# Kernel optimization log

Hardware: AMD Instinct MI355X
Metric: run time of the kernel (lower is better)

The kernel has to match this reference:

```python
import jax, jax.numpy as jnp
import numpy as np

N = 50000      # nodes
E = 800000     # edges
D = 128        # input_dim
HID = 128      # hidden_dim
OUT = 128      # output_dim
NH = 16        # n_heads (head_dim = 8)
EF = 16        # edge_feat_dim
RF = 64        # r_feat_dim
KV = 2 * D + EF + RF  # 336


def _ln(x, g, b):
    m = x.mean(-1, keepdims=True)
    v = ((x - m) ** 2).mean(-1, keepdims=True)
    return (x - m) / jnp.sqrt(v + 1e-5) * g + b


def _mlp(x, W1, b1, g, be, W2, b2):
    # Linear -> LayerNorm -> ReLU -> Linear (targetdiff-style MLP, norm=True)
    h = jax.nn.relu(_ln(x @ W1 + b1, g, be))
    return h @ W2 + b2


def setup_inputs() -> dict:
    key = jax.random.key(0)
    ks = jax.random.split(key, 32)

    def w(k, shape, fan_in):
        return (jax.random.normal(k, shape, jnp.float32) / np.sqrt(fan_in)).astype(jnp.float32)

    inp = {
        'h': jax.random.normal(ks[0], (N, D), jnp.float32),
        'rel_x': jax.random.normal(ks[1], (E, 3), jnp.float32),
        'r_feat': jax.random.normal(ks[2], (E, RF), jnp.float32),
        'edge_feat': jax.random.normal(ks[3], (E, EF), jnp.float32),
        'edge_index': jax.random.randint(ks[4], (2, E), 0, N, jnp.int64 if jax.config.jax_enable_x64 else jnp.int32),
        # xk MLP: KV -> HID -> OUT
        'xk_W1': w(ks[5], (KV, HID), KV), 'xk_b1': jnp.zeros((HID,), jnp.float32),
        'xk_g': jnp.ones((HID,), jnp.float32), 'xk_be': jnp.zeros((HID,), jnp.float32),
        'xk_W2': w(ks[6], (HID, OUT), HID), 'xk_b2': jnp.zeros((OUT,), jnp.float32),
        # xv MLP: KV -> HID -> NH
        'xv_W1': w(ks[7], (KV, HID), KV), 'xv_b1': jnp.zeros((HID,), jnp.float32),
        'xv_g': jnp.ones((HID,), jnp.float32), 'xv_be': jnp.zeros((HID,), jnp.float32),
        'xv_W2': w(ks[8], (HID, NH), HID), 'xv_b2': jnp.zeros((NH,), jnp.float32),
        # xq MLP: D -> HID -> OUT
        'xq_W1': w(ks[9], (D, HID), D), 'xq_b1': jnp.zeros((HID,), jnp.float32),
        'xq_g': jnp.ones((HID,), jnp.float32), 'xq_be': jnp.zeros((HID,), jnp.float32),
        'xq_W2': w(ks[10], (HID, OUT), HID), 'xq_b2': jnp.zeros((OUT,), jnp.float32),
        # edge-weight net: Linear(RF,1) + sigmoid
        'ew_W': w(ks[11], (RF, 1), RF), 'ew_b': jnp.zeros((1,), jnp.float32),
    }
    return inp


def reference(h, rel_x, r_feat, edge_feat, edge_index,
              xk_W1, xk_b1, xk_g, xk_be, xk_W2, xk_b2,
              xv_W1, xv_b1, xv_g, xv_be, xv_W2, xv_b2,
              xq_W1, xq_b1, xq_g, xq_be, xq_W2, xq_b2,
              ew_W, ew_b):
    src, dst = edge_index[0], edge_index[1]
    # gather -> MLPs
    kv_input = jnp.concatenate([edge_feat, r_feat, h[dst], h[src]], axis=-1)  # [E, KV]
    k = _mlp(kv_input, xk_W1, xk_b1, xk_g, xk_be, xk_W2, xk_b2).reshape(-1, NH, OUT // NH)
    v = _mlp(kv_input, xv_W1, xv_b1, xv_g, xv_be, xv_W2, xv_b2)              # [E, NH]
    e_w = jax.nn.sigmoid(r_feat @ ew_W + ew_b)                               # [E, 1]
    v = v * e_w
    v = v[:, :, None] * rel_x[:, None, :]                                    # [E, NH, 3]
    q = _mlp(h, xq_W1, xq_b1, xq_g, xq_be, xq_W2, xq_b2).reshape(-1, NH, OUT // NH)
    # scatter-softmax over dst segments
    s = (q[dst] * k).sum(-1) / np.sqrt(OUT // NH)                            # [E, NH]
    smax = jax.ops.segment_max(s, dst, num_segments=N)
    ex = jnp.exp(s - smax[dst])
    den = jax.ops.segment_sum(ex, dst, num_segments=N)
    alpha = ex / den[dst]                                                     # [E, NH]
    m = alpha[:, :, None] * v                                                 # [E, NH, 3]
    out = jax.ops.segment_sum(m, dst, num_segments=N)                         # [N, NH, 3]
    return out.mean(1)                                                        # [N, 3]
```

## Files before the change

### kernel.cpp

```cpp
#include <hip/hip_runtime.h>
#include <hip/hip_bf16.h>

#define NN 50000
#define NE 800000
#define DD 128
#define NHD 16
#define EFD 16
#define RFD 64
#define KVD 336
#define KP  352
#define KST 360
#define ME 64
#define HPAD 132

typedef __attribute__((ext_vector_type(8))) short bf16x8;
typedef __attribute__((ext_vector_type(4))) float f32x4;

__device__ __forceinline__ unsigned short f2bf(float f) {
    __hip_bfloat16 h = __float2bfloat16(f);
    return __builtin_bit_cast(unsigned short, h);
}
__device__ __forceinline__ float bf2f(unsigned short u) {
    return __uint_as_float(((unsigned)u) << 16);
}

__global__ __launch_bounds__(256) void prep_wt(
    const float* __restrict__ xkW1, const float* __restrict__ xvW1,
    unsigned short* __restrict__ Wt)
{
    const int n = blockIdx.x;
    const float* W = (n < 128) ? xkW1 : xvW1;
    const int col = n & 127;
    for (int k = threadIdx.x; k < KST; k += 256) {
        float v = (k < KVD) ? W[(size_t)k * 128 + col] : 0.0f;
        Wt[(size_t)n * KST + k] = f2bf(v);
    }
}

__global__ __launch_bounds__(256) void prep_hbf(
    const float* __restrict__ h, unsigned short* __restrict__ hb)
{
    const size_t i = ((size_t)blockIdx.x * 256 + threadIdx.x) * 4;
    const float4 f = *(const float4*)&h[i];
    ushort4 o;
    o.x = f2bf(f.x); o.y = f2bf(f.y); o.z = f2bf(f.z); o.w = f2bf(f.w);
    *(ushort4*)&hb[i] = o;
}

__global__ __launch_bounds__(128) void qmlp_kernel(
    const float* __restrict__ h,
    const float* __restrict__ W1, const float* __restrict__ b1,
    const float* __restrict__ g,  const float* __restrict__ be,
    const float* __restrict__ W2, const float* __restrict__ b2,
    unsigned short* __restrict__ q_bf)
{
    __shared__ float hs[4][DD];
    __shared__ float hid[4][DD];
    __shared__ float red[4][2][2];
    const int j  = threadIdx.x;
    const int n0 = blockIdx.x * 4;

    #pragma unroll
    for (int n = 0; n < 4; n++) hs[n][j] = h[(size_t)(n0 + n) * DD + j];
    __syncthreads();

    float a[4];
    #pragma unroll
    for (int n = 0; n < 4; n++) a[n] = b1[j];
    #pragma unroll 8
    for (int i = 0; i < DD; i++) {
        float w = W1[i * DD + j];
        #pragma unroll
        for (int n = 0; n < 4; n++) a[n] = fmaf(hs[n][i], w, a[n]);
    }

    const int wid = j >> 6;
    #pragma unroll
    for (int n = 0; n < 4; n++) {
        float s1 = a[n], s2 = a[n] * a[n];
        #pragma unroll
        for (int off = 32; off > 0; off >>= 1) {
            s1 += __shfl_xor(s1, off);
            s2 += __shfl_xor(s2, off);
        }
        if ((j & 63) == 0) { red[n][0][wid] = s1; red[n][1][wid] = s2; }
    }
    __syncthreads();

    const float gg = g[j], bb = be[j];
    #pragma unroll
    for (int n = 0; n < 4; n++) {
        float s1   = red[n][0][0] + red[n][0][1];
        float s2   = red[n][1][0] + red[n][1][1];
        float mean = s1 * (1.0f / DD);
        float var  = s2 * (1.0f / DD) - mean * mean;
        float r    = (a[n] - mean) * rsqrtf(var + 1e-5f) * gg + bb;
        hid[n][j]  = fmaxf(r, 0.0f);
    }
    __syncthreads();

    float o[4];
    #pragma unroll
    for (int n = 0; n < 4; n++) o[n] = b2[j];
    #pragma unroll 8
    for (int i = 0; i < DD; i++) {
        float w = W2[i * DD + j];
        #pragma unroll
        for (int n = 0; n < 4; n++) o[n] = fmaf(hid[n][i], w, o[n]);
    }
    #pragma unroll
    for (int n = 0; n < 4; n++) q_bf[(size_t)(n0 + n) * DD + j] = f2bf(o[n]);
}

union SharedU {
    unsigned short kv[ME * KST];
    float hid[ME * HPAD];
};

__global__ __launch_bounds__(256, 3) void edge_kernel(
    const unsigned short* __restrict__ h_bf,
    const float* __restrict__ rel_x,
    const float* __restrict__ r_feat,
    const float* __restrict__ edge_feat,
    const int*   __restrict__ e_src,
    const int*   __restrict__ e_dst,
    const unsigned short* __restrict__ Wt,
    const float* __restrict__ xk_b1, const float* __restrict__ xk_g,
    const float* __restrict__ xk_be,
    const float* __restrict__ xk_W2, const float* __restrict__ xk_b2,
    const float* __restrict__ xv_b1, const float* __restrict__ xv_g,
    const float* __restrict__ xv_be,
    const float* __restrict__ xv_W2, const float* __restrict__ xv_b2,
    const float* __restrict__ ew_W,  const float* __restrict__ ew_b,
    const unsigned short* __restrict__ q_bf,
    float* __restrict__ accN)
{
    __shared__ SharedU u;
    __shared__ float v_s[ME][NHD];
    __shared__ float ew_s[ME];
    __shared__ float rel_s[ME][3];
    __shared__ int   dst_s[ME];
    __shared__ int   src_s[ME];

    const int tid = threadIdx.x;
    const int e0  = blockIdx.x * ME;

    if (tid < ME) { dst_s[tid] = e_dst[e0 + tid]; src_s[tid] = e_src[e0 + tid]; }
    else {
        int t = tid - ME;
        rel_s[t / 3][t % 3] = rel_x[(size_t)e0 * 3 + t];
    }
    __syncthreads();

    {
        const int e = tid >> 2, p = tid & 3;
        const size_t ge = (size_t)(e0 + e);
        {
            float4 f = *(const float4*)&edge_feat[ge * EFD + p * 4];
            ushort4 o; o.x = f2bf(f.x); o.y = f2bf(f.y); o.z = f2bf(f.z); o.w = f2bf(f.w);
            *(ushort4*)&u.kv[e * KST + p * 4] = o;
        }
        {
            float part = 0.0f;
            #pragma unroll
            for (int i = 0; i < 4; i++) {
                float4 f = *(const float4*)&r_feat[ge * RFD + p * 16 + i * 4];
                float4 w = *(const float4*)&ew_W[p * 16 + i * 4];
                part += f.x * w.x + f.y * w.y + f.z * w.z + f.w * w.w;
                ushort4 o; o.x = f2bf(f.x); o.y = f2bf(f.y); o.z = f2bf(f.z); o.w = f2bf(f.w);
                *(ushort4*)&u.kv[e * KST + 16 + p * 16 + i * 4] = o;
            }
            part += __shfl_xor(part, 1);
            part += __shfl_xor(part, 2);
            if (p == 0) ew_s[e] = 1.0f / (1.0f + expf(-(part + ew_b[0])));
        }
        {
            const uint4* hp = (const uint4*)&h_bf[(size_t)dst_s[e] * DD + p * 32];
            uint4* op = (uint4*)&u.kv[e * KST + 80 + p * 32];
            #pragma unroll
            for (int i = 0; i < 4; i++) op[i] = hp[i];
        }
        {
            const uint4* hp = (const uint4*)&h_bf[(size_t)src_s[e] * DD + p * 32];
            uint4* op = (uint4*)&u.kv[e * KST + 208 + p * 32];
            #pragma unroll
            for (int i = 0; i < 4; i++) op[i] = hp[i];
        }
        if (p < 2) {
            uint4 z = make_uint4(0, 0, 0, 0);
            *(uint4*)&u.kv[e * KST + 336 + p * 8] = z;
        }
    }
    __syncthreads();

    const int lane = tid & 63;
    const int wv   = tid >> 6;
    const int half = wv >> 1;
    const int mrow = (wv & 1) * 32;
    const int c15  = lane & 15;
    const int q    = lane >> 4;

    f32x4 acc[2][8];
    #pragma unroll
    for (int mt = 0; mt < 2; mt++)
        #pragma unroll
        for (int nt = 0; nt < 8; nt++) acc[mt][nt] = (f32x4){0.f, 0.f, 0.f, 0.f};

    {
        const unsigned short* WtH = Wt + (size_t)(half * 128 + c15) * KST;
        const unsigned short* kvA = &u.kv[(mrow + c15) * KST];
        for (int ks = 0; ks < 11; ks++) {
            const int k0 = ks * 32 + q * 8;
            bf16x8 a0 = *(const bf16x8*)&kvA[k0];
            bf16x8 a1 = *(const bf16x8*)&kvA[16 * KST + k0];
            #pragma unroll
            for (int nt = 0; nt < 8; nt++) {
                bf16x8 b = *(const bf16x8*)&WtH[(size_t)nt * 16 * KST + k0];
                acc[0][nt] = __builtin_amdgcn_mfma_f32_16x16x32_bf16(a0, b, acc[0][nt], 0, 0, 0);
                acc[1][nt] = __builtin_amdgcn_mfma_f32_16x16x32_bf16(a1, b, acc[1][nt], 0, 0, 0);
            }
        }
    }

    {
        const float* b1p = half ? xv_b1 : xk_b1;
        const float* gp  = half ? xv_g  : xk_g;
        const float* bep = half ? xv_be : xk_be;
        float bia[8], gam[8], bet[8];
        #pragma unroll
        for (int nt = 0; nt < 8; nt++) {
            int idx = nt * 16 + c15;
            bia[nt] = b1p[idx]; gam[nt] = gp[idx]; bet[nt] = bep[idx];
        }
        #pragma unroll
        for (int mt = 0; mt < 2; mt++)
            #pragma unroll
            for (int r = 0; r < 4; r++) {
                float x[8]; float s1 = 0.f, s2 = 0.f;
                #pragma unroll
                for (int nt = 0; nt < 8; nt++) {
                    x[nt] = acc[mt][nt][r] + bia[nt];
                    s1 += x[nt]; s2 = fmaf(x[nt], x[nt], s2);
                }
                #pragma unroll
                for (int off = 1; off < 16; off <<= 1) {
                    s1 += __shfl_xor(s1, off);
                    s2 += __shfl_xor(s2, off);
                }
                float mean = s1 * (1.0f / 128.0f);
                float var  = s2 * (1.0f / 128.0f) - mean * mean;
                float rstd = rsqrtf(var + 1e-5f);
                #pragma unroll
                for (int nt = 0; nt < 8; nt++)
                    acc[mt][nt][r] = fmaxf((x[nt] - mean) * rstd * gam[nt] + bet[nt], 0.0f);
            }
    }
    __syncthreads();

    if (half == 0) {
        #pragma unroll
        for (int mt = 0; mt < 2; mt++)
            #pragma unroll
            for (int r = 0; r < 4; r++)
                #pragma unroll
                for (int nt = 0; nt < 8; nt++)
                    u.hid[(mrow + mt * 16 + q * 4 + r) * HPAD + nt * 16 + c15] = acc[mt][nt][r];
    }
    __syncthreads();

    const int tc2 = tid & 31;
    const int te2 = tid >> 5;
    float k_acc[8][4];
    {
        const float4 b2v = *(const float4*)&xk_b2[tc2 * 4];
        #pragma unroll
        for (int e = 0; e < 8; e++) {
            k_acc[e][0] = b2v.x; k_acc[e][1] = b2v.y;
            k_acc[e][2] = b2v.z; k_acc[e][3] = b2v.w;
        }
        #pragma unroll 4
        for (int i4 = 0; i4 < 32; i4++) {
            const float4 w0 = *(const float4*)&xk_W2[(i4 * 4 + 0) * 128 + tc2 * 4];
            const float4 w1 = *(const float4*)&xk_W2[(i4 * 4 + 1) * 128 + tc2 * 4];
            const float4 w2 = *(const float4*)&xk_W2[(i4 * 4 + 2) * 128 + tc2 * 4];
            const float4 w3 = *(const float4*)&xk_W2[(i4 * 4 + 3) * 128 + tc2 * 4];
            #pragma unroll
            for (int e = 0; e < 8; e++) {
                const float4 hv = *(const float4*)&u.hid[(te2 * 8 + e) * HPAD + i4 * 4];
                k_acc[e][0] = fmaf(hv.x, w0.x, k_acc[e][0]);
                k_acc[e][1] = fmaf(hv.x, w0.y, k_acc[e][1]);
                k_acc[e][2] = fmaf(hv.x, w0.z, k_acc[e][2]);
                k_acc[e][3] = fmaf(hv.x, w0.w, k_acc[e][3]);
                k_acc[e][0] = fmaf(hv.y, w1.x, k_acc[e][0]);
                k_acc[e][1] = fmaf(hv.y, w1.y, k_acc[e][1]);
                k_acc[e][2] = fmaf(hv.y, w1.z, k_acc[e][2]);
                k_acc[e][3] = fmaf(hv.y, w1.w, k_acc[e][3]);
                k_acc[e][0] = fmaf(hv.z, w2.x, k_acc[e][0]);
                k_acc[e][1] = fmaf(hv.z, w2.y, k_acc[e][1]);
                k_acc[e][2] = fmaf(hv.z, w2.z, k_acc[e][2]);
                k_acc[e][3] = fmaf(hv.z, w2.w, k_acc[e][3]);
                k_acc[e][0] = fmaf(hv.w, w3.x, k_acc[e][0]);
                k_acc[e][1] = fmaf(hv.w, w3.y, k_acc[e][1]);
                k_acc[e][2] = fmaf(hv.w, w3.z, k_acc[e][2]);
                k_acc[e][3] = fmaf(hv.w, w3.w, k_acc[e][3]);
            }
        }
    }
    __syncthreads();

    if (half == 1) {
        #pragma unroll
        for (int mt = 0; mt < 2; mt++)
            #pragma unroll
            for (int r = 0; r < 4; r++)
                #pragma unroll
                for (int nt = 0; nt < 8; nt++)
                    u.hid[(mrow + mt * 16 + q * 4 + r) * HPAD + nt * 16 + c15] = acc[mt][nt][r];
    }
    __syncthreads();

    #pragma unroll
    for (int p = 0; p < 4; p++) {
        int item = tid + p * 256;
        int e    = item >> 4;
        int col  = item & 15;
        float a = xv_b2[col];
        #pragma unroll 8
        for (int i4 = 0; i4 < 32; i4++) {
            const float4 hv = *(const float4*)&u.hid[e * HPAD + i4 * 4];
            a = fmaf(hv.x, xv_W2[(i4 * 4 + 0) * 16 + col], a);
            a = fmaf(hv.y, xv_W2[(i4 * 4 + 1) * 16 + col], a);
            a = fmaf(hv.z, xv_W2[(i4 * 4 + 2) * 16 + col], a);
            a = fmaf(hv.w, xv_W2[(i4 * 4 + 3) * 16 + col], a);
        }
        v_s[e][col] = a;
    }
    __syncthreads();

    {
        const float inv_s8 = 0.35355339059327373f;
        const int head = tc2 >> 1;
        const int sub  = tc2 & 1;
        #pragma unroll
        for (int e = 0; e < 8; e++) {
            int el  = te2 * 8 + e;
            int dst = dst_s[el];
            const ushort4 qb = *(const ushort4*)&q_bf[(size_t)dst * DD + tc2 * 4];
            float p = bf2f(qb.x) * k_acc[e][0] + bf2f(qb.y) * k_acc[e][1] +
                      bf2f(qb.z) * k_acc[e][2] + bf2f(qb.w) * k_acc[e][3];
            p += __shfl_xor(p, 1);
            if (sub == 0) {
                float ex = expf(p * inv_s8);
                float vw = v_s[el][head] * ew_s[el] * ex;
                float* base = &accN[(((size_t)dst * NHD) + head) * 4];
                atomicAdd(base + 0, vw * rel_s[el][0]);
                atomicAdd(base + 1, vw * rel_s[el][1]);
                atomicAdd(base + 2, vw * rel_s[el][2]);
                atomicAdd(base + 3, ex);
            }
        }
    }
}

__global__ __launch_bounds__(256) void finalize_kernel(
    const float* __restrict__ accN, float* __restrict__ out)
{
    int n = blockIdx.x * blockDim.x + threadIdx.x;
    if (n >= NN) return;
    float ox = 0.0f, oy = 0.0f, oz = 0.0f;
    #pragma unroll
    for (int hh = 0; hh < NHD; hh++) {
        float4 a = *(const float4*)&accN[(((size_t)n * NHD) + hh) * 4];
        if (a.w > 0.0f) {
            float r = 1.0f / a.w;
            ox = fmaf(a.x, r, ox);
            oy = fmaf(a.y, r, oy);
            oz = fmaf(a.z, r, oz);
        }
    }
    out[n * 3 + 0] = ox * (1.0f / NHD);
    out[n * 3 + 1] = oy * (1.0f / NHD);
    out[n * 3 + 2] = oz * (1.0f / NHD);
}

extern "C" void kernel_launch(void* const* d_in, const int* in_sizes, int n_in,
                              void* d_out, int out_size, void* d_ws, size_t ws_size,
                              hipStream_t stream)
{
    const float* h         = (const float*)d_in[0];
    const float* rel_x     = (const float*)d_in[1];
    const float* r_feat    = (const float*)d_in[2];
    const float* edge_feat = (const float*)d_in[3];
    const int*   e_idx     = (const int*)d_in[4];
    const float* xk_W1 = (const float*)d_in[5];
    const float* xk_b1 = (const float*)d_in[6];
    const float* xk_g  = (const float*)d_in[7];
    const float* xk_be = (const float*)d_in[8];
    const float* xk_W2 = (const float*)d_in[9];
    const float* xk_b2 = (const float*)d_in[10];
    const float* xv_W1 = (const float*)d_in[11];
    const float* xv_b1 = (const float*)d_in[12];
    const float* xv_g  = (const float*)d_in[13];
    const float* xv_be = (const float*)d_in[14];
    const float* xv_W2 = (const float*)d_in[15];
    const float* xv_b2 = (const float*)d_in[16];
    const float* xq_W1 = (const float*)d_in[17];
    const float* xq_b1 = (const float*)d_in[18];
    const float* xq_g  = (const float*)d_in[19];
    const float* xq_be = (const float*)d_in[20];
    const float* xq_W2 = (const float*)d_in[21];
    const float* xq_b2 = (const float*)d_in[22];
    const float* ew_W  = (const float*)d_in[23];
    const float* ew_b  = (const float*)d_in[24];

    float* accN = (float*)d_ws;
    unsigned short* h_bf = (unsigned short*)(accN + (size_t)NN * NHD * 4);
    unsigned short* q_bf = h_bf + (size_t)NN * DD;
    unsigned short* Wt   = q_bf + (size_t)NN * DD;

    hipMemsetAsync(accN, 0, (size_t)NN * NHD * 4 * sizeof(float), stream);

    prep_hbf<<<(NN * DD / 4 + 255) / 256, 256, 0, stream>>>(h, h_bf);
    prep_wt<<<256, 256, 0, stream>>>(xk_W1, xv_W1, Wt);

    qmlp_kernel<<<NN / 4, 128, 0, stream>>>(h, xq_W1, xq_b1, xq_g, xq_be,
                                            xq_W2, xq_b2, q_bf);

    edge_kernel<<<NE / ME, 256, 0, stream>>>(
        h_bf, rel_x, r_feat, edge_feat,
        e_idx, e_idx + NE,
        Wt,
        xk_b1, xk_g, xk_be, xk_W2, xk_b2,
        xv_b1, xv_g, xv_be, xv_W2, xv_b2,
        ew_W, ew_b, q_bf, accN);

    finalize_kernel<<<(NN + 255) / 256, 256, 0, stream>>>(accN, (float*)d_out);
}
```

Before: 1.652 ms.

## Compute xk second linear layer with bf16 MFMA instead of scalar FMAs

The hidden activations for the k and v MLPs are now stored to shared memory as bf16 in separate buffers, so both are written at once and the two-phase store/sync sequence goes away. The 128x128 second k layer now runs on MFMA 16x16x32 bf16 instructions, with a pre-transposed bf16 copy of xk_W2 built by a new prep kernel. k results go through shared memory for the attention-score step. This removes a large scalar FP32 FMA loop but adds bf16 rounding of the hidden activations and an extra shared-memory round trip.

```diff
diff --git a/kernel.cpp b/kernel.cpp
--- a/kernel.cpp
+++ b/kernel.cpp
@@ -8,10 +8,10 @@
 #define EFD 16
 #define RFD 64
 #define KVD 336
-#define KP  352
 #define KST 360
 #define ME 64
-#define HPAD 132
+#define HST 136
+#define KSS 132
 
 typedef __attribute__((ext_vector_type(8))) short bf16x8;
 typedef __attribute__((ext_vector_type(4))) float f32x4;
@@ -35,6 +35,17 @@
         float v = (k < KVD) ? W[(size_t)k * 128 + col] : 0.0f;
         Wt[(size_t)n * KST + k] = f2bf(v);
     }
+}
+
+__global__ __launch_bounds__(128) void prep_wt2(
+    const float* __restrict__ xkW2, const float* __restrict__ xvW2,
+    unsigned short* __restrict__ Wt2)
+{
+    const int n = blockIdx.x;
+    const int k = threadIdx.x;
+    float v = (n < 128) ? xkW2[(size_t)k * 128 + n]
+                        : xvW2[(size_t)k * 16 + (n - 128)];
+    Wt2[(size_t)n * 128 + k] = f2bf(v);
 }
 
 __global__ __launch_bounds__(256) void prep_hbf(
@@ -114,7 +125,11 @@
 
 union SharedU {
     unsigned short kv[ME * KST];
-    float hid[ME * HPAD];
+    struct {
+        unsigned short hidk[ME * HST];
+        unsigned short hidv[ME * HST];
+    } s2;
+    float ks[ME * KSS];
 };
 
 __global__ __launch_bounds__(256, 3) void edge_kernel(
@@ -125,18 +140,18 @@
     const int*   __restrict__ e_src,
     const int*   __restrict__ e_dst,
     const unsigned short* __restrict__ Wt,
+    const unsigned short* __restrict__ Wt2,
     const float* __restrict__ xk_b1, const float* __restrict__ xk_g,
-    const float* __restrict__ xk_be,
-    const float* __restrict__ xk_W2, const float* __restrict__ xk_b2,
+    const float* __restrict__ xk_be, const float* __restrict__ xk_b2,
     const float* __restrict__ xv_b1, const float* __restrict__ xv_g,
-    const float* __restrict__ xv_be,
-    const float* __restrict__ xv_W2, const float* __restrict__ xv_b2,
+    const float* __restrict__ xv_be, const float* __restrict__ xv_W2,
+    const float* __restrict__ xv_b2,
     const float* __restrict__ ew_W,  const float* __restrict__ ew_b,
     const unsigned short* __restrict__ q_bf,
     float* __restrict__ accN)
 {
     __shared__ SharedU u;
-    __shared__ float v_s[ME][NHD];
+    __shared__ float v_s[ME][NHD + 1];
     __shared__ float ew_s[ME];
     __shared__ float rel_s[ME][3];
     __shared__ int   dst_s[ME];
@@ -257,68 +272,46 @@
     }
     __syncthreads();
 
-    if (half == 0) {
+    {
+        unsigned short* hdst = half ? u.s2.hidv : u.s2.hidk;
         #pragma unroll
         for (int mt = 0; mt < 2; mt++)
             #pragma unroll
-            for (int r = 0; r < 4; r++)
+            for (int r = 0; r < 4; r++) {
+                const int row = mrow + mt * 16 + q * 4 + r;
                 #pragma unroll
                 for (int nt = 0; nt < 8; nt++)
-                    u.hid[(mrow + mt * 16 + q * 4 + r) * HPAD + nt * 16 + c15] = acc[mt][nt][r];
-    }
-    __syncthreads();
-
-    const int tc2 = tid & 31;
-    const int te2 = tid >> 5;
-    float k_acc[8][4];
-    {
-        const float4 b2v = *(const float4*)&xk_b2[tc2 * 4];
-        #pragma unroll
-        for (int e = 0; e < 8; e++) {
-            k_acc[e][0] = b2v.x; k_acc[e][1] = b2v.y;
-            k_acc[e][2] = b2v.z; k_acc[e][3] = b2v.w;
-        }
-        #pragma unroll 4
-        for (int i4 = 0; i4 < 32; i4++) {
-            const float4 w0 = *(const float4*)&xk_W2[(i4 * 4 + 0) * 128 + tc2 * 4];
-            const float4 w1 = *(const float4*)&xk_W2[(i4 * 4 + 1) * 128 + tc2 * 4];
-            const float4 w2 = *(const float4*)&xk_W2[(i4 * 4 + 2) * 128 + tc2 * 4];
-            const float4 w3 = *(const float4*)&xk_W2[(i4 * 4 + 3) * 128 + tc2 * 4];
-            #pragma unroll
-            for (int e = 0; e < 8; e++) {
-                const float4 hv = *(const float4*)&u.hid[(te2 * 8 + e) * HPAD + i4 * 4];
-                k_acc[e][0] = fmaf(hv.x, w0.x, k_acc[e][0]);
-                k_acc[e][1] = fmaf(hv.x, w0.y, k_acc[e][1]);
-                k_acc[e][2] = fmaf(hv.x, w0.z, k_acc[e][2]);
-                k_acc[e][3] = fmaf(hv.x, w0.w, k_acc[e][3]);
-                k_acc[e][0] = fmaf(hv.y, w1.x, k_acc[e][0]);
-                k_acc[e][1] = fmaf(hv.y, w1.y, k_acc[e][1]);
-                k_acc[e][2] = fmaf(hv.y, w1.z, k_acc[e][2]);
-                k_acc[e][3] = fmaf(hv.y, w1.w, k_acc[e][3]);
-                k_acc[e][0] = fmaf(hv.z, w2.x, k_acc[e][0]);
-                k_acc[e][1] = fmaf(hv.z, w2.y, k_acc[e][1]);
-                k_acc[e][2] = fmaf(hv.z, w2.z, k_acc[e][2]);
-                k_acc[e][3] = fmaf(hv.z, w2.w, k_acc[e][3]);
-                k_acc[e][0] = fmaf(hv.w, w3.x, k_acc[e][0]);
-                k_acc[e][1] = fmaf(hv.w, w3.y, k_acc[e][1]);
-                k_acc[e][2] = fmaf(hv.w, w3.z, k_acc[e][2]);
-                k_acc[e][3] = fmaf(hv.w, w3.w, k_acc[e][3]);
-            }
-        }
-    }
-    __syncthreads();
-
-    if (half == 1) {
-        #pragma unroll
-        for (int mt = 0; mt < 2; mt++)
-            #pragma unroll
-            for (int r = 0; r < 4; r++)
-                #pragma unroll
-                for (int nt = 0; nt < 8; nt++)
-                    u.hid[(mrow + mt * 16 + q * 4 + r) * HPAD + nt * 16 + c15] = acc[mt][nt][r];
-    }
-    __syncthreads();
-
+                    hdst[row * HST + nt * 16 + c15] = f2bf(acc[mt][nt][r]);
+            }
+    }
+    __syncthreads();
+
+    const int mb2 = (wv & 1) * 32;
+    const int nb2 = (wv >> 1) * 64;
+    f32x4 acck[2][4];
+    #pragma unroll
+    for (int mt = 0; mt < 2; mt++)
+        #pragma unroll
+        for (int nt = 0; nt < 4; nt++) acck[mt][nt] = (f32x4){0.f, 0.f, 0.f, 0.f};
+    {
+        const unsigned short* A0 = &u.s2.hidk[(mb2 + c15) * HST];
+        const unsigned short* A1 = &u.s2.hidk[(mb2 + 16 + c15) * HST];
+        const unsigned short* B0 = &Wt2[(size_t)(nb2 + c15) * 128];
+        #pragma unroll
+        for (int ks = 0; ks < 4; ks++) {
+            const int k0 = ks * 32 + q * 8;
+            bf16x8 a0 = *(const bf16x8*)&A0[k0];
+            bf16x8 a1 = *(const bf16x8*)&A1[k0];
+            #pragma unroll
+            for (int nt = 0; nt < 4; nt++) {
+                bf16x8 b = *(const bf16x8*)&B0[(size_t)nt * 16 * 128 + k0];
+                acck[0][nt] = __builtin_amdgcn_mfma_f32_16x16x32_bf16(a0, b, acck[0][nt], 0, 0, 0);
+                acck[1][nt] = __builtin_amdgcn_mfma_f32_16x16x32_bf16(a1, b, acck[1][nt], 0, 0, 0);
+            }
+        }
+    }
+
+    float vacc[4];
     #pragma unroll
     for (int p = 0; p < 4; p++) {
         int item = tid + p * 256;
@@ -327,27 +320,47 @@
         float a = xv_b2[col];
         #pragma unroll 8
         for (int i4 = 0; i4 < 32; i4++) {
-            const float4 hv = *(const float4*)&u.hid[e * HPAD + i4 * 4];
-            a = fmaf(hv.x, xv_W2[(i4 * 4 + 0) * 16 + col], a);
-            a = fmaf(hv.y, xv_W2[(i4 * 4 + 1) * 16 + col], a);
-            a = fmaf(hv.z, xv_W2[(i4 * 4 + 2) * 16 + col], a);
-            a = fmaf(hv.w, xv_W2[(i4 * 4 + 3) * 16 + col], a);
-        }
-        v_s[e][col] = a;
+            const ushort4 hv = *(const ushort4*)&u.s2.hidv[e * HST + i4 * 4];
+            a = fmaf(bf2f(hv.x), xv_W2[(i4 * 4 + 0) * 16 + col], a);
+            a = fmaf(bf2f(hv.y), xv_W2[(i4 * 4 + 1) * 16 + col], a);
+            a = fmaf(bf2f(hv.z), xv_W2[(i4 * 4 + 2) * 16 + col], a);
+            a = fmaf(bf2f(hv.w), xv_W2[(i4 * 4 + 3) * 16 + col], a);
+        }
+        vacc[p] = a;
+    }
+    __syncthreads();
+
+    #pragma unroll
+    for (int nt = 0; nt < 4; nt++) {
+        const float bias = xk_b2[nb2 + nt * 16 + c15];
+        #pragma unroll
+        for (int mt = 0; mt < 2; mt++)
+            #pragma unroll
+            for (int r = 0; r < 4; r++)
+                u.ks[(mb2 + mt * 16 + q * 4 + r) * KSS + nb2 + nt * 16 + c15] =
+                    acck[mt][nt][r] + bias;
+    }
+    #pragma unroll
+    for (int p = 0; p < 4; p++) {
+        int item = tid + p * 256;
+        v_s[item >> 4][item & 15] = vacc[p];
     }
     __syncthreads();
 
     {
         const float inv_s8 = 0.35355339059327373f;
+        const int tc2  = tid & 31;
+        const int te2  = tid >> 5;
         const int head = tc2 >> 1;
         const int sub  = tc2 & 1;
         #pragma unroll
         for (int e = 0; e < 8; e++) {
             int el  = te2 * 8 + e;
             int dst = dst_s[el];
+            const float4  kk = *(const float4*)&u.ks[el * KSS + tc2 * 4];
             const ushort4 qb = *(const ushort4*)&q_bf[(size_t)dst * DD + tc2 * 4];
-            float p = bf2f(qb.x) * k_acc[e][0] + bf2f(qb.y) * k_acc[e][1] +
-                      bf2f(qb.z) * k_acc[e][2] + bf2f(qb.w) * k_acc[e][3];
+            float p = bf2f(qb.x) * kk.x + bf2f(qb.y) * kk.y +
+                      bf2f(qb.z) * kk.z + bf2f(qb.w) * kk.w;
             p += __shfl_xor(p, 1);
             if (sub == 0) {
                 float ex = expf(p * inv_s8);
@@ -417,11 +430,13 @@
     unsigned short* h_bf = (unsigned short*)(accN + (size_t)NN * NHD * 4);
     unsigned short* q_bf = h_bf + (size_t)NN * DD;
     unsigned short* Wt   = q_bf + (size_t)NN * DD;
+    unsigned short* Wt2  = Wt + (size_t)256 * KST;
 
     hipMemsetAsync(accN, 0, (size_t)NN * NHD * 4 * sizeof(float), stream);
 
     prep_hbf<<<(NN * DD / 4 + 255) / 256, 256, 0, stream>>>(h, h_bf);
     prep_wt<<<256, 256, 0, stream>>>(xk_W1, xv_W1, Wt);
+    prep_wt2<<<144, 128, 0, stream>>>(xk_W2, xv_W2, Wt2);
 
     qmlp_kernel<<<NN / 4, 128, 0, stream>>>(h, xq_W1, xq_b1, xq_g, xq_be,
                                             xq_W2, xq_b2, q_bf);
@@ -429,8 +444,8 @@
     edge_kernel<<<NE / ME, 256, 0, stream>>>(
         h_bf, rel_x, r_feat, edge_feat,
         e_idx, e_idx + NE,
-        Wt,
-        xk_b1, xk_g, xk_be, xk_W2, xk_b2,
+        Wt, Wt2,
+        xk_b1, xk_g, xk_be, xk_b2,
         xv_b1, xv_g, xv_be, xv_W2, xv_b2,
         ew_W, ew_b, q_bf, accN);
 
```

After: 1.423 ms. -13.9%, faster.
